# Kernel optimization log

Hardware: AMD Instinct MI355X
Metric: run time of the kernel (lower is better)

Reference implementation:

```python
import jax, jax.numpy as jnp
import numpy as np

B, T, C, I, E, K, V, H = 4, 512, 512, 2048, 32, 2, 32000, 8
D = C // H
EPS = 1e-5


def setup_inputs() -> dict:
    key = jax.random.key(0)
    ks = jax.random.split(key, 16)
    s = 0.02
    inp = {
        "input_ids": jax.random.randint(ks[0], (B, T), 0, V),
        "emb": jax.random.normal(ks[1], (V, C), jnp.float32) * s,
        "wq": jax.random.normal(ks[2], (C, C), jnp.float32) * s,
        "wk": jax.random.normal(ks[3], (C, C), jnp.float32) * s,
        "wv": jax.random.normal(ks[4], (C, C), jnp.float32) * s,
        "wo": jax.random.normal(ks[5], (C, C), jnp.float32) * s,
        "gate": jax.random.normal(ks[6], (C, E), jnp.float32) * s,
        "w1": jax.random.normal(ks[7], (E, C, I), jnp.float32) * s,
        "w2": jax.random.normal(ks[8], (E, I, C), jnp.float32) * s,
        "g1": jnp.ones((C,), jnp.float32) + jax.random.normal(ks[9], (C,), jnp.float32) * 0.01,
        "b1": jax.random.normal(ks[10], (C,), jnp.float32) * 0.01,
        "g2": jnp.ones((C,), jnp.float32) + jax.random.normal(ks[11], (C,), jnp.float32) * 0.01,
        "b2": jax.random.normal(ks[12], (C,), jnp.float32) * 0.01,
        "lm_head": jax.random.normal(ks[13], (C, V), jnp.float32) * s,
    }
    return inp


def _ln(x, g, b):
    mu = jnp.mean(x, axis=-1, keepdims=True)
    var = jnp.mean(jnp.square(x - mu), axis=-1, keepdims=True)
    return (x - mu) * jax.lax.rsqrt(var + EPS) * g + b


def reference(input_ids, emb, wq, wk, wv, wo, gate, w1, w2, g1, b1, g2, b2, lm_head):
    h = emb[input_ids]  # [B,T,C]
    # --- attention block ---
    x = _ln(h, g1, b1)
    q = (x @ wq).reshape(B, T, H, D).transpose(0, 2, 1, 3)  # [B,H,T,D]
    k = (x @ wk).reshape(B, T, H, D).transpose(0, 2, 1, 3)
    v = (x @ wv).reshape(B, T, H, D).transpose(0, 2, 1, 3)
    scores = jnp.einsum('bhqd,bhkd->bhqk', q, k) / jnp.sqrt(jnp.float32(D))
    causal = jnp.tril(jnp.ones((T, T), bool))
    scores = jnp.where(causal, scores, jnp.finfo(scores.dtype).min)
    attn = jax.nn.softmax(scores, axis=-1)
    ao = jnp.einsum('bhqk,bhkd->bhqd', attn, v)
    ao = ao.transpose(0, 2, 1, 3).reshape(B, T, C) @ wo
    h = h + ao
    # --- MoE block ---
    x2 = _ln(h, g2, b2)          # hidden_states_for_moe [B,T,C]
    flat = x2.reshape(-1, C)     # [N,C], N = B*T tokens
    router_logits = flat @ gate  # [N,E]
    rw, sel = jax.lax.top_k(router_logits, K)   # [N,K]
    rw = jax.nn.softmax(rw.astype(jnp.float32), axis=-1)
    # dense per-expert FFN, then mask to selected experts (same math as
    # torch's loop: unselected (token,expert) slots stay zero)
    hidden = jax.nn.gelu(jnp.einsum('tc,eci->tei', flat, w1), approximate=False)
    all_out = jnp.einsum('tei,eic->tec', hidden, w2)  # [N,E,C]
    sel_mask = jnp.sum(jax.nn.one_hot(sel, E, dtype=all_out.dtype), axis=1)  # [N,E]
    full_expert_outputs = all_out * sel_mask[:, :, None]
    gathered = jnp.take_along_axis(full_expert_outputs, sel[:, :, None], axis=1)  # [N,K,C]
    moe_out = jnp.einsum('tk,tkc->tc', rw, gathered).reshape(B, T, C)
    h = h + moe_out
    logits = h @ lm_head
    return logits, full_expert_outputs, router_logits, x2
```

## Files before the change

kernel.cpp:

```cpp
#include <hip/hip_runtime.h>
#include <hip/hip_bf16.h>

#define BATCH 4
#define SEQ   512
#define CH    512
#define NTOK  2048
#define FF    2048
#define NEXP  32
#define TOPK  2
#define VOCAB 32000
#define NHEAD 8
#define HDIM  64
#define EPSF  1e-5f

typedef __attribute__((ext_vector_type(8))) short short8v;
typedef __attribute__((ext_vector_type(4))) float f32x4;

#define GLD16(g, lds) __builtin_amdgcn_global_load_lds(                      \
    (const __attribute__((address_space(1))) void*)(g),                      \
    (__attribute__((address_space(3))) void*)(lds), 16, 0, 0)

__device__ __forceinline__ unsigned short bf16r(float f) {
  unsigned int u = __float_as_uint(f);
  u = (u + 0x7FFFu + ((u >> 16) & 1u)) >> 16;
  return (unsigned short)u;
}

__device__ __forceinline__ float block_reduce_sum(float v, float* sbuf) {
  #pragma unroll
  for (int off = 32; off > 0; off >>= 1) v += __shfl_down(v, off, 64);
  const int lane = threadIdx.x & 63, wid = threadIdx.x >> 6;
  __syncthreads();
  if (lane == 0) sbuf[wid] = v;
  __syncthreads();
  return sbuf[0] + sbuf[1] + sbuf[2] + sbuf[3];
}

__device__ __forceinline__ float gelu_exact(float v) {
  return 0.5f * v * (1.f + erff(v * 0.70710678118654752f));
}

__global__ __launch_bounds__(256) void transpose_cvt_kernel(
    const float* __restrict__ in, unsigned short* __restrict__ out, int R, int C) {
  __shared__ float T[64][65];
  const size_t zoff = (size_t)blockIdx.z * R * C;
  in += zoff; out += zoff;
  const int r0 = blockIdx.y << 6;
  const int c0 = blockIdx.x << 6;
  const int t = threadIdx.x;
  const int lr = t >> 4;
  const int lc = (t & 15) << 2;
  #pragma unroll
  for (int rr = 0; rr < 64; rr += 16) {
    const float4 v = *(const float4*)(in + (size_t)(r0 + lr + rr) * C + c0 + lc);
    T[lr + rr][lc + 0] = v.x; T[lr + rr][lc + 1] = v.y;
    T[lr + rr][lc + 2] = v.z; T[lr + rr][lc + 3] = v.w;
  }
  __syncthreads();
  const int oc = t >> 2;
  const int rs = (t & 3) << 4;
  unsigned int pk[8];
  #pragma unroll
  for (int j = 0; j < 8; ++j) {
    const float a = T[rs + 2 * j][oc];
    const float b = T[rs + 2 * j + 1][oc];
    pk[j] = (unsigned int)bf16r(a) | ((unsigned int)bf16r(b) << 16);
  }
  unsigned short* op = out + (size_t)(c0 + oc) * R + r0 + rs;
  *(uint4*)(op)     = make_uint4(pk[0], pk[1], pk[2], pk[3]);
  *(uint4*)(op + 8) = make_uint4(pk[4], pk[5], pk[6], pk[7]);
}

__global__ __launch_bounds__(256) void embed_ln_kernel(
    const int* __restrict__ ids, const float* __restrict__ emb,
    const float* __restrict__ g, const float* __restrict__ b,
    float* __restrict__ h, float* __restrict__ x) {
  __shared__ float sbuf[4];
  const int n = blockIdx.x, t = threadIdx.x;
  const float2 v = *(const float2*)(emb + (size_t)ids[n] * CH + 2 * t);
  *(float2*)(h + (size_t)n * CH + 2 * t) = v;
  const float mu = block_reduce_sum(v.x + v.y, sbuf) * (1.f / CH);
  const float d0 = v.x - mu, d1 = v.y - mu;
  const float var = block_reduce_sum(d0 * d0 + d1 * d1, sbuf) * (1.f / CH);
  const float rstd = rsqrtf(var + EPSF);
  const float2 gg = *(const float2*)(g + 2 * t);
  const float2 bb = *(const float2*)(b + 2 * t);
  *(float2*)(x + (size_t)n * CH + 2 * t) =
      make_float2(d0 * rstd * gg.x + bb.x, d1 * rstd * gg.y + bb.y);
}

__global__ __launch_bounds__(256) void ln2_kernel(
    const float* __restrict__ in, const float* __restrict__ g,
    const float* __restrict__ b, float* __restrict__ outf,
    unsigned short* __restrict__ outbf) {
  __shared__ float sbuf[4];
  const int n = blockIdx.x, t = threadIdx.x;
  const float2 v = *(const float2*)(in + (size_t)n * CH + 2 * t);
  const float mu = block_reduce_sum(v.x + v.y, sbuf) * (1.f / CH);
  const float d0 = v.x - mu, d1 = v.y - mu;
  const float var = block_reduce_sum(d0 * d0 + d1 * d1, sbuf) * (1.f / CH);
  const float rstd = rsqrtf(var + EPSF);
  const float2 gg = *(const float2*)(g + 2 * t);
  const float2 bb = *(const float2*)(b + 2 * t);
  const float o0 = d0 * rstd * gg.x + bb.x;
  const float o1 = d1 * rstd * gg.y + bb.y;
  *(float2*)(outf + (size_t)n * CH + 2 * t) = make_float2(o0, o1);
  ((unsigned int*)outbf)[(size_t)n * (CH / 2) + t] =
      (unsigned int)bf16r(o0) | ((unsigned int)bf16r(o1) << 16);
}

__global__ __launch_bounds__(256) void gemm_f32_qkv_kernel(
    const float* __restrict__ A,
    const float* __restrict__ Wq, const float* __restrict__ Wk,
    const float* __restrict__ Wv,
    float* __restrict__ Oq, float* __restrict__ Ok, float* __restrict__ Ov,
    int M, int N, int K) {
  const float* B = (blockIdx.z == 0) ? Wq : (blockIdx.z == 1) ? Wk : Wv;
  float*       C = (blockIdx.z == 0) ? Oq : (blockIdx.z == 1) ? Ok : Ov;
  __shared__ float As[32][68];
  __shared__ float Bs[32][132];
  const int m0 = blockIdx.y << 6;
  const int n0 = blockIdx.x << 7;
  const int t  = threadIdx.x;
  const int tm = t >> 4;
  const int tn = t & 15;
  float acc[4][8];
  #pragma unroll
  for (int i = 0; i < 4; ++i)
    #pragma unroll
    for (int j = 0; j < 8; ++j) acc[i][j] = 0.f;

  const int ar = t >> 3;
  const int ac = (t & 7) << 2;
  const int bk = t >> 3;
  const int bn = (t & 7) << 4;

  for (int kt = 0; kt < K; kt += 32) {
    #pragma unroll
    for (int rr = 0; rr < 64; rr += 32) {
      float4 a = *(const float4*)(A + (size_t)(m0 + ar + rr) * K + kt + ac);
      As[ac + 0][ar + rr] = a.x; As[ac + 1][ar + rr] = a.y;
      As[ac + 2][ar + rr] = a.z; As[ac + 3][ar + rr] = a.w;
    }
    const float* bp = B + (size_t)(kt + bk) * N + n0 + bn;
    #pragma unroll
    for (int j = 0; j < 16; j += 4)
      *(float4*)&Bs[bk][bn + j] = *(const float4*)(bp + j);
    __syncthreads();
    #pragma unroll
    for (int k = 0; k < 32; ++k) {
      const float4 av = *(const float4*)&As[k][tm << 2];
      const float4 bl = *(const float4*)&Bs[k][tn << 2];
      const float4 bh = *(const float4*)&Bs[k][64 + (tn << 2)];
      const float a_[4] = {av.x, av.y, av.z, av.w};
      const float b_[8] = {bl.x, bl.y, bl.z, bl.w, bh.x, bh.y, bh.z, bh.w};
      #pragma unroll
      for (int i = 0; i < 4; ++i)
        #pragma unroll
        for (int j = 0; j < 8; ++j)
          acc[i][j] = fmaf(a_[i], b_[j], acc[i][j]);
    }
    __syncthreads();
  }
  #pragma unroll
  for (int i = 0; i < 4; ++i) {
    const int row = m0 + (tm << 2) + i;
    float* cp = C + (size_t)row * N + n0 + (tn << 2);
    *(float4*)cp        = make_float4(acc[i][0], acc[i][1], acc[i][2], acc[i][3]);
    *(float4*)(cp + 64) = make_float4(acc[i][4], acc[i][5], acc[i][6], acc[i][7]);
  }
}

__global__ __launch_bounds__(256) void gemm_f32_kernel(
    const float* __restrict__ A, const float* __restrict__ B,
    const float* __restrict__ Res, float* __restrict__ C,
    int M, int N, int K) {
  __shared__ float As[32][68];
  __shared__ float Bs[32][132];
  const int m0 = blockIdx.y << 6;
  const int n0 = blockIdx.x << 7;
  const int t  = threadIdx.x;
  const int tm = t >> 4;
  const int tn = t & 15;
  float acc[4][8];
  #pragma unroll
  for (int i = 0; i < 4; ++i)
    #pragma unroll
    for (int j = 0; j < 8; ++j) acc[i][j] = 0.f;

  const int ar = t >> 3;
  const int ac = (t & 7) << 2;
  const int bk = t >> 3;
  const int bn = (t & 7) << 4;

  for (int kt = 0; kt < K; kt += 32) {
    #pragma unroll
    for (int rr = 0; rr < 64; rr += 32) {
      float4 a = *(const float4*)(A + (size_t)(m0 + ar + rr) * K + kt + ac);
      As[ac + 0][ar + rr] = a.x; As[ac + 1][ar + rr] = a.y;
      As[ac + 2][ar + rr] = a.z; As[ac + 3][ar + rr] = a.w;
    }
    const float* bp = B + (size_t)(kt + bk) * N + n0 + bn;
    #pragma unroll
    for (int j = 0; j < 16; j += 4)
      *(float4*)&Bs[bk][bn + j] = *(const float4*)(bp + j);
    __syncthreads();
    #pragma unroll
    for (int k = 0; k < 32; ++k) {
      const float4 av = *(const float4*)&As[k][tm << 2];
      const float4 bl = *(const float4*)&Bs[k][tn << 2];
      const float4 bh = *(const float4*)&Bs[k][64 + (tn << 2)];
      const float a_[4] = {av.x, av.y, av.z, av.w};
      const float b_[8] = {bl.x, bl.y, bl.z, bl.w, bh.x, bh.y, bh.z, bh.w};
      #pragma unroll
      for (int i = 0; i < 4; ++i)
        #pragma unroll
        for (int j = 0; j < 8; ++j)
          acc[i][j] = fmaf(a_[i], b_[j], acc[i][j]);
    }
    __syncthreads();
  }
  #pragma unroll
  for (int i = 0; i < 4; ++i) {
    const int row = m0 + (tm << 2) + i;
    float* cp = C + (size_t)row * N + n0 + (tn << 2);
    float4 lo = make_float4(acc[i][0], acc[i][1], acc[i][2], acc[i][3]);
    float4 hi = make_float4(acc[i][4], acc[i][5], acc[i][6], acc[i][7]);
    if (Res) {
      const float* rp = Res + (size_t)row * N + n0 + (tn << 2);
      const float4 r0 = *(const float4*)rp;
      const float4 r1 = *(const float4*)(rp + 64);
      lo.x += r0.x; lo.y += r0.y; lo.z += r0.z; lo.w += r0.w;
      hi.x += r1.x; hi.y += r1.y; hi.z += r1.z; hi.w += r1.w;
    }
    *(float4*)cp        = lo;
    *(float4*)(cp + 64) = hi;
  }
}

template <int SWZ>
__global__ __launch_bounds__(256) void gemm_bf16_kernel(
    const unsigned short* __restrict__ A, const unsigned short* __restrict__ BT,
    float* __restrict__ C, int M, int N, int K) {
  int bx = blockIdx.x, by = blockIdx.y;
  if (SWZ) {
    const int gx = gridDim.x;
    const int nb = gx * gridDim.y;
    int bid = by * gx + bx;
    bid = (bid & 7) * (nb >> 3) + (bid >> 3);
    bx = bid % gx;
    by = bid / gx;
  }
  __shared__ unsigned short As[128][64];
  __shared__ unsigned short Bs[128][64];
  const int m0 = by << 7;
  const int n0 = bx << 7;
  const int t  = threadIdx.x;
  const int w  = t >> 6;
  const int l  = t & 63;
  const int wm = (w >> 1) << 6;
  const int wn = (w & 1) << 6;
  const int fr = l & 15;
  const int fg = l >> 4;
  const int lrow = l >> 3;
  const int lcol = (l & 7) << 3;
  f32x4 acc[4][4];
  #pragma unroll
  for (int i = 0; i < 4; ++i)
    #pragma unroll
    for (int j = 0; j < 4; ++j) acc[i][j] = (f32x4){0.f, 0.f, 0.f, 0.f};

  for (int kt = 0; kt < K; kt += 64) {
    #pragma unroll
    for (int q = 0; q < 4; ++q) {
      const int r = (w << 5) + (q << 3);
      GLD16(A  + (size_t)(m0 + r + lrow) * K + kt + lcol, &As[r][0]);
      GLD16(BT + (size_t)(n0 + r + lrow) * K + kt + lcol, &Bs[r][0]);
    }
    __syncthreads();
    #pragma unroll
    for (int kk = 0; kk < 64; kk += 32) {
      short8v afr[4], bfr[4];
      #pragma unroll
      for (int i = 0; i < 4; ++i)
        afr[i] = *(const short8v*)&As[wm + (i << 4) + fr][kk + (fg << 3)];
      #pragma unroll
      for (int j = 0; j < 4; ++j)
        bfr[j] = *(const short8v*)&Bs[wn + (j << 4) + fr][kk + (fg << 3)];
      #pragma unroll
      for (int i = 0; i < 4; ++i)
        #pragma unroll
        for (int j = 0; j < 4; ++j)
          acc[i][j] = __builtin_amdgcn_mfma_f32_16x16x32_bf16(afr[i], bfr[j], acc[i][j], 0, 0, 0);
    }
    __syncthreads();
  }
  #pragma unroll
  for (int i = 0; i < 4; ++i) {
    #pragma unroll
    for (int j = 0; j < 4; ++j) {
      const int col = n0 + wn + (j << 4) + fr;
      const int rowb = m0 + wm + (i << 4) + (fg << 2);
      #pragma unroll
      for (int r = 0; r < 4; ++r)
        C[(size_t)(rowb + r) * N + col] = acc[i][j][r];
    }
  }
}

__global__ __launch_bounds__(256) void attn_kernel(
    const float* __restrict__ q, const float* __restrict__ kbuf,
    const float* __restrict__ vbuf, float* __restrict__ ao) {
  __shared__ float Ks[64][68];
  __shared__ float Vs[64][68];
  __shared__ float Sx[64][65];
  const int bh = blockIdx.x;
  const int qt = blockIdx.y;
  const int b  = bh >> 3;
  const int hh = bh & 7;
  const int t  = threadIdx.x;
  const int qi   = t >> 2;
  const int part = t & 3;
  const int qglob = (qt << 6) + qi;
  const size_t qoff = (size_t)(b * SEQ + qglob) * CH + hh * HDIM + (part << 4);
  float qreg[16];
  #pragma unroll
  for (int j = 0; j < 16; j += 4) {
    const float4 v4 = *(const float4*)(q + qoff + j);
    qreg[j] = v4.x; qreg[j + 1] = v4.y; qreg[j + 2] = v4.z; qreg[j + 3] = v4.w;
  }
  float o[16];
  #pragma unroll
  for (int j = 0; j < 16; ++j) o[j] = 0.f;
  float m = -3.0e38f, l = 0.f;
  const int lr = t >> 2;
  const int lc = (t & 3) << 4;
  for (int kt = 0; kt <= qt; ++kt) {
    const size_t base = (size_t)(b * SEQ + (kt << 6) + lr) * CH + hh * HDIM + lc;
    #pragma unroll
    for (int j = 0; j < 16; j += 4) {
      *(float4*)&Ks[lr][lc + j] = *(const float4*)(kbuf + base + j);
      *(float4*)&Vs[lr][lc + j] = *(const float4*)(vbuf + base + j);
    }
    __syncthreads();
    float sloc[16];
    float tmax = -3.0e38f;
    for (int kk = 0; kk < 64; ++kk) {
      float p = 0.f;
      const float* kr = &Ks[kk][part << 4];
      #pragma unroll
      for (int j = 0; j < 16; ++j) p = fmaf(qreg[j], kr[j], p);
      p += __shfl_xor(p, 1, 64);
      p += __shfl_xor(p, 2, 64);
      p *= 0.125f;
      if (((kt << 6) + kk) > qglob) p = -3.0e38f;
      tmax = fmaxf(tmax, p);
      if ((kk & 3) == part) sloc[kk >> 2] = p;
    }
    const float mnew = fmaxf(m, tmax);
    const float corr = expf(m - mnew);
    float lsum = 0.f;
    #pragma unroll
    for (int j = 0; j < 16; ++j) {
      const float pe = expf(sloc[j] - mnew);
      lsum += pe;
      Sx[qi][(j << 2) + part] = pe;
    }
    lsum += __shfl_xor(lsum, 1, 64);
    lsum += __shfl_xor(lsum, 2, 64);
    l = l * corr + lsum;
    m = mnew;
    #pragma unroll
    for (int j = 0; j < 16; ++j) o[j] *= corr;
    __syncthreads();
    for (int kk = 0; kk < 64; ++kk) {
      const float pv = Sx[qi][kk];
      const float* vr = &Vs[kk][part << 4];
      #pragma unroll
      for (int j = 0; j < 16; ++j) o[j] = fmaf(pv, vr[j], o[j]);
    }
    __syncthreads();
  }
  const float inv = 1.f / l;
  #pragma unroll
  for (int j = 0; j < 16; j += 4)
    *(float4*)(ao + qoff + j) =
        make_float4(o[j] * inv, o[j + 1] * inv, o[j + 2] * inv, o[j + 3] * inv);
}

__global__ __launch_bounds__(256) void router_kernel(
    const float* __restrict__ x2, const float* __restrict__ gate,
    float* __restrict__ rl, float* __restrict__ rw, int* __restrict__ sel,
    int* __restrict__ counts, int* __restrict__ lists) {
  __shared__ float xrow[CH];
  __shared__ float lg[NEXP];
  const int n = blockIdx.x;
  const int t = threadIdx.x;
  xrow[t]       = x2[(size_t)n * CH + t];
  xrow[t + 256] = x2[(size_t)n * CH + t + 256];
  __syncthreads();
  const int e = t >> 3, i = t & 7;
  float p = 0.f;
  const float* gp = gate + e;
  for (int c = i * 64; c < i * 64 + 64; ++c) p = fmaf(xrow[c], gp[(size_t)c * NEXP], p);
  p += __shfl_xor(p, 1, 64);
  p += __shfl_xor(p, 2, 64);
  p += __shfl_xor(p, 4, 64);
  if (i == 0) { lg[e] = p; rl[(size_t)n * NEXP + e] = p; }
  __syncthreads();
  if (t == 0) {
    int i0 = 0; float v0 = lg[0];
    for (int j = 1; j < NEXP; ++j) if (lg[j] > v0) { v0 = lg[j]; i0 = j; }
    int i1 = (i0 == 0) ? 1 : 0; float v1 = lg[i1];
    for (int j = 0; j < NEXP; ++j) {
      if (j == i0 || j == i1) continue;
      if (lg[j] > v1) { v1 = lg[j]; i1 = j; }
    }
    const float ex = expf(v1 - v0);
    const float den = 1.f + ex;
    rw[n * 2]     = 1.f / den;
    rw[n * 2 + 1] = ex / den;
    sel[n * 2]     = i0;
    sel[n * 2 + 1] = i1;
    const int s0 = atomicAdd(&counts[i0], 1);
    lists[i0 * NTOK + s0] = n * 2;
    const int s1 = atomicAdd(&counts[i1], 1);
    lists[i1 * NTOK + s1] = n * 2 + 1;
  }
}

__global__ __launch_bounds__(256) void moe_fc1_bf16(
    const unsigned short* __restrict__ x2bf, const unsigned short* __restrict__ w1T,
    const int* __restrict__ counts, const int* __restrict__ lists,
    unsigned short* __restrict__ hidden) {
  const int e  = blockIdx.y;
  const int nt = counts[e];
  const int mt = blockIdx.z << 6;
  if (mt >= nt) return;
  const int i0 = blockIdx.x << 7;
  __shared__ unsigned short As[64][72];
  __shared__ unsigned short Bs[128][64];
  __shared__ int ls[64];
  const int* lst = lists + e * NTOK;
  const int t = threadIdx.x;
  if (t < 64) ls[t] = (mt + t < nt) ? lst[mt + t] : -1;
  __syncthreads();
  const int w  = t >> 6, l = t & 63;
  const int wm = (w >> 1) << 5;
  const int wn = (w & 1) << 6;
  const int fr = l & 15, fg = l >> 4;
  const int lrow = l >> 3, lcol = (l & 7) << 3;
  f32x4 acc[2][4];
  #pragma unroll
  for (int i = 0; i < 2; ++i)
    #pragma unroll
    for (int j = 0; j < 4; ++j) acc[i][j] = (f32x4){0.f, 0.f, 0.f, 0.f};

  const int arow = t >> 2, akc = (t & 3) << 4;
  const int apid = ls[arow];
  const unsigned short* arp = (apid >= 0) ? (x2bf + (size_t)(apid >> 1) * CH) : nullptr;
  const unsigned short* w1e = w1T + (size_t)e * FF * CH;

  for (int kt = 0; kt < CH; kt += 64) {
    if (arp) {
      *(uint4*)&As[arow][akc + 0] = *(const uint4*)(arp + kt + akc + 0);
      *(uint4*)&As[arow][akc + 8] = *(const uint4*)(arp + kt + akc + 8);
    } else {
      *(uint4*)&As[arow][akc + 0] = make_uint4(0, 0, 0, 0);
      *(uint4*)&As[arow][akc + 8] = make_uint4(0, 0, 0, 0);
    }
    #pragma unroll
    for (int q = 0; q < 4; ++q) {
      const int r = (w << 5) + (q << 3);
      GLD16(w1e + (size_t)(i0 + r + lrow) * CH + kt + lcol, &Bs[r][0]);
    }
    __syncthreads();
    #pragma unroll
    for (int kk = 0; kk < 64; kk += 32) {
      short8v afr[2], bfr[4];
      #pragma unroll
      for (int i = 0; i < 2; ++i)
        afr[i] = *(const short8v*)&As[wm + (i << 4) + fr][kk + (fg << 3)];
      #pragma unroll
      for (int j = 0; j < 4; ++j)
        bfr[j] = *(const short8v*)&Bs[wn + (j << 4) + fr][kk + (fg << 3)];
      #pragma unroll
      for (int i = 0; i < 2; ++i)
        #pragma unroll
        for (int j = 0; j < 4; ++j)
          acc[i][j] = __builtin_amdgcn_mfma_f32_16x16x32_bf16(afr[i], bfr[j], acc[i][j], 0, 0, 0);
    }
    __syncthreads();
  }
  #pragma unroll
  for (int i = 0; i < 2; ++i) {
    #pragma unroll
    for (int r = 0; r < 4; ++r) {
      const int lrow2 = wm + (i << 4) + (fg << 2) + r;
      const int pid = ls[lrow2];
      if (pid < 0) continue;
      unsigned short* hp = hidden + (size_t)pid * FF + i0 + wn + fr;
      #pragma unroll
      for (int j = 0; j < 4; ++j)
        hp[j << 4] = bf16r(gelu_exact(acc[i][j][r]));
    }
  }
}

__global__ __launch_bounds__(256) void moe_fc2_bf16(
    const unsigned short* __restrict__ hidden, const unsigned short* __restrict__ w2T,
    const int* __restrict__ counts, const int* __restrict__ lists,
    float* __restrict__ fe) {
  const int e  = blockIdx.y;
  const int nt = counts[e];
  const int mt = blockIdx.z << 6;
  if (mt >= nt) return;
  const int c0 = blockIdx.x << 7;
  __shared__ unsigned short As[64][72];
  __shared__ unsigned short Bs[128][64];
  __shared__ int ls[64];
  const int* lst = lists + e * NTOK;
  const int t = threadIdx.x;
  if (t < 64) ls[t] = (mt + t < nt) ? lst[mt + t] : -1;
  __syncthreads();
  const int w  = t >> 6, l = t & 63;
  const int wm = (w >> 1) << 5;
  const int wn = (w & 1) << 6;
  const int fr = l & 15, fg = l >> 4;
  const int lrow = l >> 3, lcol = (l & 7) << 3;
  f32x4 acc[2][4];
  #pragma unroll
  for (int i = 0; i < 2; ++i)
    #pragma unroll
    for (int j = 0; j < 4; ++j) acc[i][j] = (f32x4){0.f, 0.f, 0.f, 0.f};

  const int arow = t >> 2, akc = (t & 3) << 4;
  const int apid = ls[arow];
  const unsigned short* arp = (apid >= 0) ? (hidden + (size_t)apid * FF) : nullptr;
  const unsigned short* w2e = w2T + (size_t)e * CH * FF;

  for (int kt = 0; kt < FF; kt += 64) {
    if (arp) {
      *(uint4*)&As[arow][akc + 0] = *(const uint4*)(arp + kt + akc + 0);
      *(uint4*)&As[arow][akc + 8] = *(const uint4*)(arp + kt + akc + 8);
    } else {
      *(uint4*)&As[arow][akc + 0] = make_uint4(0, 0, 0, 0);
      *(uint4*)&As[arow][akc + 8] = make_uint4(0, 0, 0, 0);
    }
    #pragma unroll
    for (int q = 0; q < 4; ++q) {
      const int r = (w << 5) + (q << 3);
      GLD16(w2e + (size_t)(c0 + r + lrow) * FF + kt + lcol, &Bs[r][0]);
    }
    __syncthreads();
    #pragma unroll
    for (int kk = 0; kk < 64; kk += 32) {
      short8v afr[2], bfr[4];
      #pragma unroll
      for (int i = 0; i < 2; ++i)
        afr[i] = *(const short8v*)&As[wm + (i << 4) + fr][kk + (fg << 3)];
      #pragma unroll
      for (int j = 0; j < 4; ++j)
        bfr[j] = *(const short8v*)&Bs[wn + (j << 4) + fr][kk + (fg << 3)];
      #pragma unroll
      for (int i = 0; i < 2; ++i)
        #pragma unroll
        for (int j = 0; j < 4; ++j)
          acc[i][j] = __builtin_amdgcn_mfma_f32_16x16x32_bf16(afr[i], bfr[j], acc[i][j], 0, 0, 0);
    }
    __syncthreads();
  }
  #pragma unroll
  for (int i = 0; i < 2; ++i) {
    #pragma unroll
    for (int r = 0; r < 4; ++r) {
      const int lrow2 = wm + (i << 4) + (fg << 2) + r;
      const int pid = ls[lrow2];
      if (pid < 0) continue;
      const int n = pid >> 1;
      float* op = fe + ((size_t)n * NEXP + e) * CH + c0 + wn + fr;
      #pragma unroll
      for (int j = 0; j < 4; ++j)
        op[j << 4] = acc[i][j][r];
    }
  }
}

__global__ __launch_bounds__(256) void combine_kernel(
    const float* __restrict__ h2, const float* __restrict__ fe,
    const float* __restrict__ rw, const int* __restrict__ sel,
    unsigned short* __restrict__ hfbf) {
  const int idx = blockIdx.x * 256 + threadIdx.x;
  const int n = idx >> 7;
  const int c = (idx & 127) << 2;
  const float w0 = rw[n * 2], w1 = rw[n * 2 + 1];
  const int s0 = sel[n * 2], s1 = sel[n * 2 + 1];
  const float* base = fe + (size_t)n * NEXP * CH + c;
  const float4 f0 = *(const float4*)(base + (size_t)s0 * CH);
  const float4 f1 = *(const float4*)(base + (size_t)s1 * CH);
  const float4 a  = *(const float4*)(h2 + (size_t)n * CH + c);
  const float ox = a.x + w0 * f0.x + w1 * f1.x;
  const float oy = a.y + w0 * f0.y + w1 * f1.y;
  const float oz = a.z + w0 * f0.z + w1 * f1.z;
  const float ow = a.w + w0 * f0.w + w1 * f1.w;
  uint2 pk;
  pk.x = (unsigned int)bf16r(ox) | ((unsigned int)bf16r(oy) << 16);
  pk.y = (unsigned int)bf16r(oz) | ((unsigned int)bf16r(ow) << 16);
  *(uint2*)(hfbf + (size_t)n * CH + c) = pk;
}

extern "C" void kernel_launch(void* const* d_in, const int* in_sizes, int n_in,
                              void* d_out, int out_size, void* d_ws, size_t ws_size,
                              hipStream_t stream) {
  const int*   ids  = (const int*)d_in[0];
  const float* emb  = (const float*)d_in[1];
  const float* wq   = (const float*)d_in[2];
  const float* wk   = (const float*)d_in[3];
  const float* wv   = (const float*)d_in[4];
  const float* wo   = (const float*)d_in[5];
  const float* gate = (const float*)d_in[6];
  const float* w1   = (const float*)d_in[7];
  const float* w2   = (const float*)d_in[8];
  const float* g1   = (const float*)d_in[9];
  const float* b1   = (const float*)d_in[10];
  const float* g2   = (const float*)d_in[11];
  const float* b2   = (const float*)d_in[12];
  const float* lmh  = (const float*)d_in[13];

  float* out        = (float*)d_out;
  float* out_logits = out;
  float* out_fe     = out_logits + (size_t)NTOK * VOCAB;
  float* out_rl     = out_fe + (size_t)NTOK * NEXP * CH;
  float* out_x2     = out_rl + (size_t)NTOK * NEXP;

  unsigned short* w1T    = (unsigned short*)(out_logits);
  unsigned short* w2T    = (unsigned short*)(out_logits + 16777216);
  unsigned short* hidden = (unsigned short*)(out_logits + 33554432);
  float*          x      = out_logits + 37748736;
  float*          qb     = out_logits + 38797312;
  float*          kb     = out_logits + 39845888;
  float*          vb     = out_logits + 40894464;
  float*          ao     = out_logits + 41943040;
  float*          h      = out_logits + 42991616;
  float*          h2     = out_logits + 44040192;
  unsigned short* x2_bf  = (unsigned short*)(out_logits + 45088768);

  float* ws    = (float*)d_ws;
  unsigned short* lmhT  = (unsigned short*)ws;
  unsigned short* hf_bf = (unsigned short*)(ws + 8192000);
  float* rw    = ws + 8716288;
  int*   sel   = (int*)(rw + NTOK * TOPK);
  int*   counts= sel + NTOK * TOPK;
  int*   lists = counts + 64;

  hipMemsetAsync(counts, 0, NEXP * sizeof(int), stream);
  hipMemsetAsync(out_fe, 0, (size_t)NTOK * NEXP * CH * sizeof(float), stream);

  transpose_cvt_kernel<<<dim3(500, 8, 1),   256, 0, stream>>>(lmh, lmhT, CH, VOCAB);
  transpose_cvt_kernel<<<dim3(32, 8, NEXP), 256, 0, stream>>>(w1, w1T, CH, FF);
  transpose_cvt_kernel<<<dim3(8, 32, NEXP), 256, 0, stream>>>(w2, w2T, FF, CH);

  embed_ln_kernel<<<NTOK, 256, 0, stream>>>(ids, emb, g1, b1, h, x);

  gemm_f32_qkv_kernel<<<dim3(CH / 128, NTOK / 64, 3), 256, 0, stream>>>(
      x, wq, wk, wv, qb, kb, vb, NTOK, CH, CH);

  attn_kernel<<<dim3(BATCH * NHEAD, SEQ / 64), 256, 0, stream>>>(qb, kb, vb, ao);

  gemm_f32_kernel<<<dim3(CH / 128, NTOK / 64), 256, 0, stream>>>(ao, wo, h, h2, NTOK, CH, CH);

  ln2_kernel<<<NTOK, 256, 0, stream>>>(h2, g2, b2, out_x2, x2_bf);

  router_kernel<<<NTOK, 256, 0, stream>>>(out_x2, gate, out_rl, rw, sel, counts, lists);

  moe_fc1_bf16<<<dim3(FF / 128, NEXP, NTOK / 64), 256, 0, stream>>>(x2_bf, w1T, counts, lists, hidden);
  moe_fc2_bf16<<<dim3(CH / 128, NEXP, NTOK / 64), 256, 0, stream>>>(hidden, w2T, counts, lists, out_fe);

  combine_kernel<<<dim3(NTOK * CH / 1024), 256, 0, stream>>>(h2, out_fe, rw, sel, hf_bf);

  gemm_bf16_kernel<1><<<dim3(VOCAB / 128, NTOK / 128), 256, 0, stream>>>(
      hf_bf, lmhT, out_logits, NTOK, VOCAB, CH);
}
```

Baseline: 1.178 ms.

## Fuse LN2 with router, widen attention blocks, stage LM-head stores via LDS

LayerNorm2 and the router are merged into one kernel that keeps the normalized row in shared memory, which removes a launch and a global re-read of x2. The attention kernel now uses 512 threads with 8 lanes per query instead of 4, for more parallelism and fewer registers per thread, and it drops one barrier. The bf16 LM-head GEMM now writes its output through an LDS staging buffer so the fp32 stores are coalesced float4 writes. The cost is extra shared memory and barriers in the GEMM epilogue, and a third shuffle step in attention.

```diff
diff --git a/kernel.cpp b/kernel.cpp
--- a/kernel.cpp
+++ b/kernel.cpp
@@ -89,11 +89,15 @@
       make_float2(d0 * rstd * gg.x + bb.x, d1 * rstd * gg.y + bb.y);
 }
 
-__global__ __launch_bounds__(256) void ln2_kernel(
+__global__ __launch_bounds__(256) void ln2_router_kernel(
     const float* __restrict__ in, const float* __restrict__ g,
-    const float* __restrict__ b, float* __restrict__ outf,
-    unsigned short* __restrict__ outbf) {
+    const float* __restrict__ b, const float* __restrict__ gate,
+    float* __restrict__ outf, unsigned short* __restrict__ outbf,
+    float* __restrict__ rl, float* __restrict__ rw, int* __restrict__ sel,
+    int* __restrict__ counts, int* __restrict__ lists) {
   __shared__ float sbuf[4];
+  __shared__ float xrow[CH];
+  __shared__ float lg[NEXP];
   const int n = blockIdx.x, t = threadIdx.x;
   const float2 v = *(const float2*)(in + (size_t)n * CH + 2 * t);
   const float mu = block_reduce_sum(v.x + v.y, sbuf) * (1.f / CH);
@@ -107,297 +111,7 @@
   *(float2*)(outf + (size_t)n * CH + 2 * t) = make_float2(o0, o1);
   ((unsigned int*)outbf)[(size_t)n * (CH / 2) + t] =
       (unsigned int)bf16r(o0) | ((unsigned int)bf16r(o1) << 16);
-}
-
-__global__ __launch_bounds__(256) void gemm_f32_qkv_kernel(
-    const float* __restrict__ A,
-    const float* __restrict__ Wq, const float* __restrict__ Wk,
-    const float* __restrict__ Wv,
-    float* __restrict__ Oq, float* __restrict__ Ok, float* __restrict__ Ov,
-    int M, int N, int K) {
-  const float* B = (blockIdx.z == 0) ? Wq : (blockIdx.z == 1) ? Wk : Wv;
-  float*       C = (blockIdx.z == 0) ? Oq : (blockIdx.z == 1) ? Ok : Ov;
-  __shared__ float As[32][68];
-  __shared__ float Bs[32][132];
-  const int m0 = blockIdx.y << 6;
-  const int n0 = blockIdx.x << 7;
-  const int t  = threadIdx.x;
-  const int tm = t >> 4;
-  const int tn = t & 15;
-  float acc[4][8];
-  #pragma unroll
-  for (int i = 0; i < 4; ++i)
-    #pragma unroll
-    for (int j = 0; j < 8; ++j) acc[i][j] = 0.f;
-
-  const int ar = t >> 3;
-  const int ac = (t & 7) << 2;
-  const int bk = t >> 3;
-  const int bn = (t & 7) << 4;
-
-  for (int kt = 0; kt < K; kt += 32) {
-    #pragma unroll
-    for (int rr = 0; rr < 64; rr += 32) {
-      float4 a = *(const float4*)(A + (size_t)(m0 + ar + rr) * K + kt + ac);
-      As[ac + 0][ar + rr] = a.x; As[ac + 1][ar + rr] = a.y;
-      As[ac + 2][ar + rr] = a.z; As[ac + 3][ar + rr] = a.w;
-    }
-    const float* bp = B + (size_t)(kt + bk) * N + n0 + bn;
-    #pragma unroll
-    for (int j = 0; j < 16; j += 4)
-      *(float4*)&Bs[bk][bn + j] = *(const float4*)(bp + j);
-    __syncthreads();
-    #pragma unroll
-    for (int k = 0; k < 32; ++k) {
-      const float4 av = *(const float4*)&As[k][tm << 2];
-      const float4 bl = *(const float4*)&Bs[k][tn << 2];
-      const float4 bh = *(const float4*)&Bs[k][64 + (tn << 2)];
-      const float a_[4] = {av.x, av.y, av.z, av.w};
-      const float b_[8] = {bl.x, bl.y, bl.z, bl.w, bh.x, bh.y, bh.z, bh.w};
-      #pragma unroll
-      for (int i = 0; i < 4; ++i)
-        #pragma unroll
-        for (int j = 0; j < 8; ++j)
-          acc[i][j] = fmaf(a_[i], b_[j], acc[i][j]);
-    }
-    __syncthreads();
-  }
-  #pragma unroll
-  for (int i = 0; i < 4; ++i) {
-    const int row = m0 + (tm << 2) + i;
-    float* cp = C + (size_t)row * N + n0 + (tn << 2);
-    *(float4*)cp        = make_float4(acc[i][0], acc[i][1], acc[i][2], acc[i][3]);
-    *(float4*)(cp + 64) = make_float4(acc[i][4], acc[i][5], acc[i][6], acc[i][7]);
-  }
-}
-
-__global__ __launch_bounds__(256) void gemm_f32_kernel(
-    const float* __restrict__ A, const float* __restrict__ B,
-    const float* __restrict__ Res, float* __restrict__ C,
-    int M, int N, int K) {
-  __shared__ float As[32][68];
-  __shared__ float Bs[32][132];
-  const int m0 = blockIdx.y << 6;
-  const int n0 = blockIdx.x << 7;
-  const int t  = threadIdx.x;
-  const int tm = t >> 4;
-  const int tn = t & 15;
-  float acc[4][8];
-  #pragma unroll
-  for (int i = 0; i < 4; ++i)
-    #pragma unroll
-    for (int j = 0; j < 8; ++j) acc[i][j] = 0.f;
-
-  const int ar = t >> 3;
-  const int ac = (t & 7) << 2;
-  const int bk = t >> 3;
-  const int bn = (t & 7) << 4;
-
-  for (int kt = 0; kt < K; kt += 32) {
-    #pragma unroll
-    for (int rr = 0; rr < 64; rr += 32) {
-      float4 a = *(const float4*)(A + (size_t)(m0 + ar + rr) * K + kt + ac);
-      As[ac + 0][ar + rr] = a.x; As[ac + 1][ar + rr] = a.y;
-      As[ac + 2][ar + rr] = a.z; As[ac + 3][ar + rr] = a.w;
-    }
-    const float* bp = B + (size_t)(kt + bk) * N + n0 + bn;
-    #pragma unroll
-    for (int j = 0; j < 16; j += 4)
-      *(float4*)&Bs[bk][bn + j] = *(const float4*)(bp + j);
-    __syncthreads();
-    #pragma unroll
-    for (int k = 0; k < 32; ++k) {
-      const float4 av = *(const float4*)&As[k][tm << 2];
-      const float4 bl = *(const float4*)&Bs[k][tn << 2];
-      const float4 bh = *(const float4*)&Bs[k][64 + (tn << 2)];
-      const float a_[4] = {av.x, av.y, av.z, av.w};
-      const float b_[8] = {bl.x, bl.y, bl.z, bl.w, bh.x, bh.y, bh.z, bh.w};
-      #pragma unroll
-      for (int i = 0; i < 4; ++i)
-        #pragma unroll
-        for (int j = 0; j < 8; ++j)
-          acc[i][j] = fmaf(a_[i], b_[j], acc[i][j]);
-    }
-    __syncthreads();
-  }
-  #pragma unroll
-  for (int i = 0; i < 4; ++i) {
-    const int row = m0 + (tm << 2) + i;
-    float* cp = C + (size_t)row * N + n0 + (tn << 2);
-    float4 lo = make_float4(acc[i][0], acc[i][1], acc[i][2], acc[i][3]);
-    float4 hi = make_float4(acc[i][4], acc[i][5], acc[i][6], acc[i][7]);
-    if (Res) {
-      const float* rp = Res + (size_t)row * N + n0 + (tn << 2);
-      const float4 r0 = *(const float4*)rp;
-      const float4 r1 = *(const float4*)(rp + 64);
-      lo.x += r0.x; lo.y += r0.y; lo.z += r0.z; lo.w += r0.w;
-      hi.x += r1.x; hi.y += r1.y; hi.z += r1.z; hi.w += r1.w;
-    }
-    *(float4*)cp        = lo;
-    *(float4*)(cp + 64) = hi;
-  }
-}
-
-template <int SWZ>
-__global__ __launch_bounds__(256) void gemm_bf16_kernel(
-    const unsigned short* __restrict__ A, const unsigned short* __restrict__ BT,
-    float* __restrict__ C, int M, int N, int K) {
-  int bx = blockIdx.x, by = blockIdx.y;
-  if (SWZ) {
-    const int gx = gridDim.x;
-    const int nb = gx * gridDim.y;
-    int bid = by * gx + bx;
-    bid = (bid & 7) * (nb >> 3) + (bid >> 3);
-    bx = bid % gx;
-    by = bid / gx;
-  }
-  __shared__ unsigned short As[128][64];
-  __shared__ unsigned short Bs[128][64];
-  const int m0 = by << 7;
-  const int n0 = bx << 7;
-  const int t  = threadIdx.x;
-  const int w  = t >> 6;
-  const int l  = t & 63;
-  const int wm = (w >> 1) << 6;
-  const int wn = (w & 1) << 6;
-  const int fr = l & 15;
-  const int fg = l >> 4;
-  const int lrow = l >> 3;
-  const int lcol = (l & 7) << 3;
-  f32x4 acc[4][4];
-  #pragma unroll
-  for (int i = 0; i < 4; ++i)
-    #pragma unroll
-    for (int j = 0; j < 4; ++j) acc[i][j] = (f32x4){0.f, 0.f, 0.f, 0.f};
-
-  for (int kt = 0; kt < K; kt += 64) {
-    #pragma unroll
-    for (int q = 0; q < 4; ++q) {
-      const int r = (w << 5) + (q << 3);
-      GLD16(A  + (size_t)(m0 + r + lrow) * K + kt + lcol, &As[r][0]);
-      GLD16(BT + (size_t)(n0 + r + lrow) * K + kt + lcol, &Bs[r][0]);
-    }
-    __syncthreads();
-    #pragma unroll
-    for (int kk = 0; kk < 64; kk += 32) {
-      short8v afr[4], bfr[4];
-      #pragma unroll
-      for (int i = 0; i < 4; ++i)
-        afr[i] = *(const short8v*)&As[wm + (i << 4) + fr][kk + (fg << 3)];
-      #pragma unroll
-      for (int j = 0; j < 4; ++j)
-        bfr[j] = *(const short8v*)&Bs[wn + (j << 4) + fr][kk + (fg << 3)];
-      #pragma unroll
-      for (int i = 0; i < 4; ++i)
-        #pragma unroll
-        for (int j = 0; j < 4; ++j)
-          acc[i][j] = __builtin_amdgcn_mfma_f32_16x16x32_bf16(afr[i], bfr[j], acc[i][j], 0, 0, 0);
-    }
-    __syncthreads();
-  }
-  #pragma unroll
-  for (int i = 0; i < 4; ++i) {
-    #pragma unroll
-    for (int j = 0; j < 4; ++j) {
-      const int col = n0 + wn + (j << 4) + fr;
-      const int rowb = m0 + wm + (i << 4) + (fg << 2);
-      #pragma unroll
-      for (int r = 0; r < 4; ++r)
-        C[(size_t)(rowb + r) * N + col] = acc[i][j][r];
-    }
-  }
-}
-
-__global__ __launch_bounds__(256) void attn_kernel(
-    const float* __restrict__ q, const float* __restrict__ kbuf,
-    const float* __restrict__ vbuf, float* __restrict__ ao) {
-  __shared__ float Ks[64][68];
-  __shared__ float Vs[64][68];
-  __shared__ float Sx[64][65];
-  const int bh = blockIdx.x;
-  const int qt = blockIdx.y;
-  const int b  = bh >> 3;
-  const int hh = bh & 7;
-  const int t  = threadIdx.x;
-  const int qi   = t >> 2;
-  const int part = t & 3;
-  const int qglob = (qt << 6) + qi;
-  const size_t qoff = (size_t)(b * SEQ + qglob) * CH + hh * HDIM + (part << 4);
-  float qreg[16];
-  #pragma unroll
-  for (int j = 0; j < 16; j += 4) {
-    const float4 v4 = *(const float4*)(q + qoff + j);
-    qreg[j] = v4.x; qreg[j + 1] = v4.y; qreg[j + 2] = v4.z; qreg[j + 3] = v4.w;
-  }
-  float o[16];
-  #pragma unroll
-  for (int j = 0; j < 16; ++j) o[j] = 0.f;
-  float m = -3.0e38f, l = 0.f;
-  const int lr = t >> 2;
-  const int lc = (t & 3) << 4;
-  for (int kt = 0; kt <= qt; ++kt) {
-    const size_t base = (size_t)(b * SEQ + (kt << 6) + lr) * CH + hh * HDIM + lc;
-    #pragma unroll
-    for (int j = 0; j < 16; j += 4) {
-      *(float4*)&Ks[lr][lc + j] = *(const float4*)(kbuf + base + j);
-      *(float4*)&Vs[lr][lc + j] = *(const float4*)(vbuf + base + j);
-    }
-    __syncthreads();
-    float sloc[16];
-    float tmax = -3.0e38f;
-    for (int kk = 0; kk < 64; ++kk) {
-      float p = 0.f;
-      const float* kr = &Ks[kk][part << 4];
-      #pragma unroll
-      for (int j = 0; j < 16; ++j) p = fmaf(qreg[j], kr[j], p);
-      p += __shfl_xor(p, 1, 64);
-      p += __shfl_xor(p, 2, 64);
-      p *= 0.125f;
-      if (((kt << 6) + kk) > qglob) p = -3.0e38f;
-      tmax = fmaxf(tmax, p);
-      if ((kk & 3) == part) sloc[kk >> 2] = p;
-    }
-    const float mnew = fmaxf(m, tmax);
-    const float corr = expf(m - mnew);
-    float lsum = 0.f;
-    #pragma unroll
-    for (int j = 0; j < 16; ++j) {
-      const float pe = expf(sloc[j] - mnew);
-      lsum += pe;
-      Sx[qi][(j << 2) + part] = pe;
-    }
-    lsum += __shfl_xor(lsum, 1, 64);
-    lsum += __shfl_xor(lsum, 2, 64);
-    l = l * corr + lsum;
-    m = mnew;
-    #pragma unroll
-    for (int j = 0; j < 16; ++j) o[j] *= corr;
-    __syncthreads();
-    for (int kk = 0; kk < 64; ++kk) {
-      const float pv = Sx[qi][kk];
-      const float* vr = &Vs[kk][part << 4];
-      #pragma unroll
-      for (int j = 0; j < 16; ++j) o[j] = fmaf(pv, vr[j], o[j]);
-    }
-    __syncthreads();
-  }
-  const float inv = 1.f / l;
-  #pragma unroll
-  for (int j = 0; j < 16; j += 4)
-    *(float4*)(ao + qoff + j) =
-        make_float4(o[j] * inv, o[j + 1] * inv, o[j + 2] * inv, o[j + 3] * inv);
-}
-
-__global__ __launch_bounds__(256) void router_kernel(
-    const float* __restrict__ x2, const float* __restrict__ gate,
-    float* __restrict__ rl, float* __restrict__ rw, int* __restrict__ sel,
-    int* __restrict__ counts, int* __restrict__ lists) {
-  __shared__ float xrow[CH];
-  __shared__ float lg[NEXP];
-  const int n = blockIdx.x;
-  const int t = threadIdx.x;
-  xrow[t]       = x2[(size_t)n * CH + t];
-  xrow[t + 256] = x2[(size_t)n * CH + t + 256];
+  xrow[2 * t] = o0; xrow[2 * t + 1] = o1;
   __syncthreads();
   const int e = t >> 3, i = t & 7;
   float p = 0.f;
@@ -427,6 +141,291 @@
     const int s1 = atomicAdd(&counts[i1], 1);
     lists[i1 * NTOK + s1] = n * 2 + 1;
   }
+}
+
+__global__ __launch_bounds__(256) void gemm_f32_qkv_kernel(
+    const float* __restrict__ A,
+    const float* __restrict__ Wq, const float* __restrict__ Wk,
+    const float* __restrict__ Wv,
+    float* __restrict__ Oq, float* __restrict__ Ok, float* __restrict__ Ov,
+    int M, int N, int K) {
+  const float* B = (blockIdx.z == 0) ? Wq : (blockIdx.z == 1) ? Wk : Wv;
+  float*       C = (blockIdx.z == 0) ? Oq : (blockIdx.z == 1) ? Ok : Ov;
+  __shared__ float As[32][68];
+  __shared__ float Bs[32][132];
+  const int m0 = blockIdx.y << 6;
+  const int n0 = blockIdx.x << 7;
+  const int t  = threadIdx.x;
+  const int tm = t >> 4;
+  const int tn = t & 15;
+  float acc[4][8];
+  #pragma unroll
+  for (int i = 0; i < 4; ++i)
+    #pragma unroll
+    for (int j = 0; j < 8; ++j) acc[i][j] = 0.f;
+
+  const int ar = t >> 3;
+  const int ac = (t & 7) << 2;
+  const int bk = t >> 3;
+  const int bn = (t & 7) << 4;
+
+  for (int kt = 0; kt < K; kt += 32) {
+    #pragma unroll
+    for (int rr = 0; rr < 64; rr += 32) {
+      float4 a = *(const float4*)(A + (size_t)(m0 + ar + rr) * K + kt + ac);
+      As[ac + 0][ar + rr] = a.x; As[ac + 1][ar + rr] = a.y;
+      As[ac + 2][ar + rr] = a.z; As[ac + 3][ar + rr] = a.w;
+    }
+    const float* bp = B + (size_t)(kt + bk) * N + n0 + bn;
+    #pragma unroll
+    for (int j = 0; j < 16; j += 4)
+      *(float4*)&Bs[bk][bn + j] = *(const float4*)(bp + j);
+    __syncthreads();
+    #pragma unroll
+    for (int k = 0; k < 32; ++k) {
+      const float4 av = *(const float4*)&As[k][tm << 2];
+      const float4 bl = *(const float4*)&Bs[k][tn << 2];
+      const float4 bh = *(const float4*)&Bs[k][64 + (tn << 2)];
+      const float a_[4] = {av.x, av.y, av.z, av.w};
+      const float b_[8] = {bl.x, bl.y, bl.z, bl.w, bh.x, bh.y, bh.z, bh.w};
+      #pragma unroll
+      for (int i = 0; i < 4; ++i)
+        #pragma unroll
+        for (int j = 0; j < 8; ++j)
+          acc[i][j] = fmaf(a_[i], b_[j], acc[i][j]);
+    }
+    __syncthreads();
+  }
+  #pragma unroll
+  for (int i = 0; i < 4; ++i) {
+    const int row = m0 + (tm << 2) + i;
+    float* cp = C + (size_t)row * N + n0 + (tn << 2);
+    *(float4*)cp        = make_float4(acc[i][0], acc[i][1], acc[i][2], acc[i][3]);
+    *(float4*)(cp + 64) = make_float4(acc[i][4], acc[i][5], acc[i][6], acc[i][7]);
+  }
+}
+
+__global__ __launch_bounds__(256) void gemm_f32_kernel(
+    const float* __restrict__ A, const float* __restrict__ B,
+    const float* __restrict__ Res, float* __restrict__ C,
+    int M, int N, int K) {
+  __shared__ float As[32][68];
+  __shared__ float Bs[32][132];
+  const int m0 = blockIdx.y << 6;
+  const int n0 = blockIdx.x << 7;
+  const int t  = threadIdx.x;
+  const int tm = t >> 4;
+  const int tn = t & 15;
+  float acc[4][8];
+  #pragma unroll
+  for (int i = 0; i < 4; ++i)
+    #pragma unroll
+    for (int j = 0; j < 8; ++j) acc[i][j] = 0.f;
+
+  const int ar = t >> 3;
+  const int ac = (t & 7) << 2;
+  const int bk = t >> 3;
+  const int bn = (t & 7) << 4;
+
+  for (int kt = 0; kt < K; kt += 32) {
+    #pragma unroll
+    for (int rr = 0; rr < 64; rr += 32) {
+      float4 a = *(const float4*)(A + (size_t)(m0 + ar + rr) * K + kt + ac);
+      As[ac + 0][ar + rr] = a.x; As[ac + 1][ar + rr] = a.y;
+      As[ac + 2][ar + rr] = a.z; As[ac + 3][ar + rr] = a.w;
+    }
+    const float* bp = B + (size_t)(kt + bk) * N + n0 + bn;
+    #pragma unroll
+    for (int j = 0; j < 16; j += 4)
+      *(float4*)&Bs[bk][bn + j] = *(const float4*)(bp + j);
+    __syncthreads();
+    #pragma unroll
+    for (int k = 0; k < 32; ++k) {
+      const float4 av = *(const float4*)&As[k][tm << 2];
+      const float4 bl = *(const float4*)&Bs[k][tn << 2];
+      const float4 bh = *(const float4*)&Bs[k][64 + (tn << 2)];
+      const float a_[4] = {av.x, av.y, av.z, av.w};
+      const float b_[8] = {bl.x, bl.y, bl.z, bl.w, bh.x, bh.y, bh.z, bh.w};
+      #pragma unroll
+      for (int i = 0; i < 4; ++i)
+        #pragma unroll
+        for (int j = 0; j < 8; ++j)
+          acc[i][j] = fmaf(a_[i], b_[j], acc[i][j]);
+    }
+    __syncthreads();
+  }
+  #pragma unroll
+  for (int i = 0; i < 4; ++i) {
+    const int row = m0 + (tm << 2) + i;
+    float* cp = C + (size_t)row * N + n0 + (tn << 2);
+    float4 lo = make_float4(acc[i][0], acc[i][1], acc[i][2], acc[i][3]);
+    float4 hi = make_float4(acc[i][4], acc[i][5], acc[i][6], acc[i][7]);
+    if (Res) {
+      const float* rp = Res + (size_t)row * N + n0 + (tn << 2);
+      const float4 r0 = *(const float4*)rp;
+      const float4 r1 = *(const float4*)(rp + 64);
+      lo.x += r0.x; lo.y += r0.y; lo.z += r0.z; lo.w += r0.w;
+      hi.x += r1.x; hi.y += r1.y; hi.z += r1.z; hi.w += r1.w;
+    }
+    *(float4*)cp        = lo;
+    *(float4*)(cp + 64) = hi;
+  }
+}
+
+template <int SWZ>
+__global__ __launch_bounds__(256) void gemm_bf16_kernel(
+    const unsigned short* __restrict__ A, const unsigned short* __restrict__ BT,
+    float* __restrict__ C, int M, int N, int K) {
+  int bx = blockIdx.x, by = blockIdx.y;
+  if (SWZ) {
+    const int gx = gridDim.x;
+    const int nb = gx * gridDim.y;
+    int bid = by * gx + bx;
+    bid = (bid & 7) * (nb >> 3) + (bid >> 3);
+    bx = bid % gx;
+    by = bid / gx;
+  }
+  __shared__ unsigned short As[128][64];
+  __shared__ unsigned short Bs[128][64];
+  __shared__ float Cs[4][16][68];
+  const int m0 = by << 7;
+  const int n0 = bx << 7;
+  const int t  = threadIdx.x;
+  const int w  = t >> 6;
+  const int l  = t & 63;
+  const int wm = (w >> 1) << 6;
+  const int wn = (w & 1) << 6;
+  const int fr = l & 15;
+  const int fg = l >> 4;
+  const int lrow = l >> 3;
+  const int lcol = (l & 7) << 3;
+  f32x4 acc[4][4];
+  #pragma unroll
+  for (int i = 0; i < 4; ++i)
+    #pragma unroll
+    for (int j = 0; j < 4; ++j) acc[i][j] = (f32x4){0.f, 0.f, 0.f, 0.f};
+
+  for (int kt = 0; kt < K; kt += 64) {
+    #pragma unroll
+    for (int q = 0; q < 4; ++q) {
+      const int r = (w << 5) + (q << 3);
+      GLD16(A  + (size_t)(m0 + r + lrow) * K + kt + lcol, &As[r][0]);
+      GLD16(BT + (size_t)(n0 + r + lrow) * K + kt + lcol, &Bs[r][0]);
+    }
+    __syncthreads();
+    #pragma unroll
+    for (int kk = 0; kk < 64; kk += 32) {
+      short8v afr[4], bfr[4];
+      #pragma unroll
+      for (int i = 0; i < 4; ++i)
+        afr[i] = *(const short8v*)&As[wm + (i << 4) + fr][kk + (fg << 3)];
+      #pragma unroll
+      for (int j = 0; j < 4; ++j)
+        bfr[j] = *(const short8v*)&Bs[wn + (j << 4) + fr][kk + (fg << 3)];
+      #pragma unroll
+      for (int i = 0; i < 4; ++i)
+        #pragma unroll
+        for (int j = 0; j < 4; ++j)
+          acc[i][j] = __builtin_amdgcn_mfma_f32_16x16x32_bf16(afr[i], bfr[j], acc[i][j], 0, 0, 0);
+    }
+    __syncthreads();
+  }
+  #pragma unroll
+  for (int i = 0; i < 4; ++i) {
+    #pragma unroll
+    for (int j = 0; j < 4; ++j)
+      #pragma unroll
+      for (int r = 0; r < 4; ++r)
+        Cs[w][(fg << 2) + r][(j << 4) + fr] = acc[i][j][r];
+    __syncthreads();
+    const int rr = l >> 2;
+    const int cc = (l & 3) << 4;
+    float* cp = C + (size_t)(m0 + wm + (i << 4) + rr) * N + n0 + wn + cc;
+    *(float4*)(cp + 0)  = *(const float4*)&Cs[w][rr][cc + 0];
+    *(float4*)(cp + 4)  = *(const float4*)&Cs[w][rr][cc + 4];
+    *(float4*)(cp + 8)  = *(const float4*)&Cs[w][rr][cc + 8];
+    *(float4*)(cp + 12) = *(const float4*)&Cs[w][rr][cc + 12];
+    __syncthreads();
+  }
+}
+
+__global__ __launch_bounds__(512) void attn_kernel(
+    const float* __restrict__ q, const float* __restrict__ kbuf,
+    const float* __restrict__ vbuf, float* __restrict__ ao) {
+  __shared__ float Ks[64][68];
+  __shared__ float Vs[64][68];
+  __shared__ float Sx[64][65];
+  const int bh = blockIdx.x;
+  const int qt = blockIdx.y;
+  const int b  = bh >> 3;
+  const int hh = bh & 7;
+  const int t  = threadIdx.x;
+  const int qi   = t >> 3;
+  const int part = t & 7;
+  const int qglob = (qt << 6) + qi;
+  const size_t qoff = (size_t)(b * SEQ + qglob) * CH + hh * HDIM + (part << 3);
+  float qreg[8];
+  {
+    const float4 a = *(const float4*)(q + qoff);
+    const float4 c = *(const float4*)(q + qoff + 4);
+    qreg[0] = a.x; qreg[1] = a.y; qreg[2] = a.z; qreg[3] = a.w;
+    qreg[4] = c.x; qreg[5] = c.y; qreg[6] = c.z; qreg[7] = c.w;
+  }
+  float o[8];
+  #pragma unroll
+  for (int j = 0; j < 8; ++j) o[j] = 0.f;
+  float m = -3.0e38f, l = 0.f;
+  const int lr = t >> 3;
+  const int lc = (t & 7) << 3;
+  for (int kt = 0; kt <= qt; ++kt) {
+    const size_t base = (size_t)(b * SEQ + (kt << 6) + lr) * CH + hh * HDIM + lc;
+    *(float4*)&Ks[lr][lc + 0] = *(const float4*)(kbuf + base + 0);
+    *(float4*)&Ks[lr][lc + 4] = *(const float4*)(kbuf + base + 4);
+    *(float4*)&Vs[lr][lc + 0] = *(const float4*)(vbuf + base + 0);
+    *(float4*)&Vs[lr][lc + 4] = *(const float4*)(vbuf + base + 4);
+    __syncthreads();
+    float sloc[8];
+    float tmax = -3.0e38f;
+    for (int kk = 0; kk < 64; ++kk) {
+      float p = 0.f;
+      const float* kr = &Ks[kk][part << 3];
+      #pragma unroll
+      for (int j = 0; j < 8; ++j) p = fmaf(qreg[j], kr[j], p);
+      p += __shfl_xor(p, 1, 64);
+      p += __shfl_xor(p, 2, 64);
+      p += __shfl_xor(p, 4, 64);
+      p *= 0.125f;
+      if (((kt << 6) + kk) > qglob) p = -3.0e38f;
+      tmax = fmaxf(tmax, p);
+      if ((kk & 7) == part) sloc[kk >> 3] = p;
+    }
+    const float mnew = fmaxf(m, tmax);
+    const float corr = expf(m - mnew);
+    float lsum = 0.f;
+    #pragma unroll
+    for (int j = 0; j < 8; ++j) {
+      const float pe = expf(sloc[j] - mnew);
+      lsum += pe;
+      Sx[qi][(j << 3) + part] = pe;
+    }
+    lsum += __shfl_xor(lsum, 1, 64);
+    lsum += __shfl_xor(lsum, 2, 64);
+    lsum += __shfl_xor(lsum, 4, 64);
+    l = l * corr + lsum;
+    m = mnew;
+    #pragma unroll
+    for (int j = 0; j < 8; ++j) o[j] *= corr;
+    for (int kk = 0; kk < 64; ++kk) {
+      const float pv = Sx[qi][kk];
+      const float* vr = &Vs[kk][part << 3];
+      #pragma unroll
+      for (int j = 0; j < 8; ++j) o[j] = fmaf(pv, vr[j], o[j]);
+    }
+    __syncthreads();
+  }
+  const float inv = 1.f / l;
+  *(float4*)(ao + qoff)     = make_float4(o[0] * inv, o[1] * inv, o[2] * inv, o[3] * inv);
+  *(float4*)(ao + qoff + 4) = make_float4(o[4] * inv, o[5] * inv, o[6] * inv, o[7] * inv);
 }
 
 __global__ __launch_bounds__(256) void moe_fc1_bf16(
@@ -665,13 +664,12 @@
   gemm_f32_qkv_kernel<<<dim3(CH / 128, NTOK / 64, 3), 256, 0, stream>>>(
       x, wq, wk, wv, qb, kb, vb, NTOK, CH, CH);
 
-  attn_kernel<<<dim3(BATCH * NHEAD, SEQ / 64), 256, 0, stream>>>(qb, kb, vb, ao);
+  attn_kernel<<<dim3(BATCH * NHEAD, SEQ / 64), 512, 0, stream>>>(qb, kb, vb, ao);
 
   gemm_f32_kernel<<<dim3(CH / 128, NTOK / 64), 256, 0, stream>>>(ao, wo, h, h2, NTOK, CH, CH);
 
-  ln2_kernel<<<NTOK, 256, 0, stream>>>(h2, g2, b2, out_x2, x2_bf);
-
-  router_kernel<<<NTOK, 256, 0, stream>>>(out_x2, gate, out_rl, rw, sel, counts, lists);
+  ln2_router_kernel<<<NTOK, 256, 0, stream>>>(h2, g2, b2, gate, out_x2, x2_bf,
+                                              out_rl, rw, sel, counts, lists);
 
   moe_fc1_bf16<<<dim3(FF / 128, NEXP, NTOK / 64), 256, 0, stream>>>(x2_bf, w1T, counts, lists, hidden);
   moe_fc2_bf16<<<dim3(CH / 128, NEXP, NTOK / 64), 256, 0, stream>>>(hidden, w2T, counts, lists, out_fe);
```

New measurement: 1.178 ms. Within noise of the previous version (+0.0%).
